# Optimization experiments

Hardware: AMD Instinct MI355X
Metric: run time of the kernel (lower is better)

## Reference

```python
import jax, jax.numpy as jnp
import numpy as np

N_NODES = 100000
N_EDGES = 1600000
D_IN = 128
D_OUT = 128


def setup_inputs() -> dict:
    key = jax.random.key(0)
    k1, k2, k3, k4, k5 = jax.random.split(key, 5)
    x = jax.random.normal(k1, (N_NODES, D_IN), dtype=jnp.float32)
    edge_row = jax.random.randint(k2, (N_EDGES,), 0, N_NODES, dtype=jnp.int32)
    edge_col = jax.random.randint(k3, (N_EDGES,), 0, N_NODES, dtype=jnp.int32)
    edge_vals = jax.random.uniform(k4, (N_EDGES,), dtype=jnp.float32)
    stdv = 1.0 / np.sqrt(D_OUT)
    weight = jax.random.uniform(k5, (D_IN, D_OUT), dtype=jnp.float32,
                                minval=-stdv, maxval=stdv)
    return {"x": x, "edge_row": edge_row, "edge_col": edge_col,
            "edge_vals": edge_vals, "weight": weight}


def reference(x, edge_row, edge_col, edge_vals, weight):
    # spmm(adj, x): gather source features, scale by edge weight, segment-sum to dst
    n = x.shape[0]
    msgs = x[edge_col] * edge_vals[:, None]          # [E, D_IN]
    agg = jax.ops.segment_sum(msgs, edge_row, num_segments=n)  # [N, D_IN]
    # dense weight matmul
    return agg @ weight                               # [N, D_OUT]
```

## Files before the change

### kernel.cpp

```cpp
#include <hip/hip_runtime.h>
#include <hip/hip_fp16.h>


#define N_NODES 100000
#define N_EDGES 1600000
#define DIM     128
#define BROWS   32
#define CB      3125
#define NSUP    49
#define LANES   8
#define NLR     (NSUP * LANES)
#define SLOT1   4608
#define SLOTCAP2 640
#define CAP     1024
#define OCAP    2048
#define CPAD    16

#define EPB1   1024
#define PBLK1  ((N_EDGES + EPB1 - 1) / EPB1)
#define CH2    1024
#define CPL    ((SLOT1 + CH2 - 1) / CH2)
#define PBLK2  (NLR * CPL)

#define OFF_CCUR1  25600000
#define OFF_CCUR2  25625088
#define OFF_OCNT   25825088
#define OFF_OBUF   25825152
#define OFF_EBUF1  25857920
#define OFF_EBUF2  40308608

__global__ __launch_bounds__(256) void gemm_xw_kernel(
    const float* __restrict__ x,
    const float* __restrict__ W,
    __half*      __restrict__ y)
{
    __shared__ __align__(16) float AsT[32 * 36];
    __shared__ float Ws[32 * 128];

    const int t    = threadIdx.x;
    const int row0 = blockIdx.x * 32;
    const int r0   = (t >> 5) * 4;
    const int c0   = (t & 31) * 4;

    float acc[4][4];
#pragma unroll
    for (int i = 0; i < 4; ++i)
#pragma unroll
        for (int j = 0; j < 4; ++j) acc[i][j] = 0.f;

    for (int k0 = 0; k0 < 128; k0 += 32) {
        {
            int r  = t >> 3;
            int kp = t & 7;
            float4 a = *(const float4*)(x + (size_t)(row0 + r) * 128 + k0 + kp * 4);
            AsT[(kp * 4 + 0) * 36 + r] = a.x;
            AsT[(kp * 4 + 1) * 36 + r] = a.y;
            AsT[(kp * 4 + 2) * 36 + r] = a.z;
            AsT[(kp * 4 + 3) * 36 + r] = a.w;
        }
        {
            const float4* Wg = (const float4*)(W + (size_t)k0 * 128);
            float4* Wl = (float4*)Ws;
#pragma unroll
            for (int i = 0; i < 4; ++i) Wl[t + 256 * i] = Wg[t + 256 * i];
        }
        __syncthreads();

#pragma unroll
        for (int kk = 0; kk < 32; ++kk) {
            float4 w = *(const float4*)(Ws + kk * 128 + c0);
            float4 a = *(const float4*)(AsT + kk * 36 + r0);
            acc[0][0] += a.x * w.x; acc[0][1] += a.x * w.y; acc[0][2] += a.x * w.z; acc[0][3] += a.x * w.w;
            acc[1][0] += a.y * w.x; acc[1][1] += a.y * w.y; acc[1][2] += a.y * w.z; acc[1][3] += a.y * w.w;
            acc[2][0] += a.z * w.x; acc[2][1] += a.z * w.y; acc[2][2] += a.z * w.z; acc[2][3] += a.z * w.w;
            acc[3][0] += a.w * w.x; acc[3][1] += a.w * w.y; acc[3][2] += a.w * w.z; acc[3][3] += a.w * w.w;
        }
        __syncthreads();
    }

#pragma unroll
    for (int i = 0; i < 4; ++i) {
        __half2 p0 = __floats2half2_rn(acc[i][0], acc[i][1]);
        __half2 p1 = __floats2half2_rn(acc[i][2], acc[i][3]);
        uint2 w;
        w.x = *(const unsigned*)&p0;
        w.y = *(const unsigned*)&p1;
        *(uint2*)(y + (size_t)(row0 + r0 + i) * 128 + c0) = w;
    }
}

__global__ __launch_bounds__(256) void zero_kernel(
    unsigned* ccur1, unsigned* ccur2, unsigned* ocnt)
{
    int i = blockIdx.x * 256 + threadIdx.x;
    if (i < NLR) ccur1[i * CPAD] = 0u;
    if (i < CB)  ccur2[i * CPAD] = 0u;
    if (i == 0)  *ocnt = 0u;
}

__global__ __launch_bounds__(256) void partition1_kernel(
    const int*   __restrict__ erow,
    const int*   __restrict__ ecol,
    const float* __restrict__ eval,
    unsigned*    __restrict__ ccur1,
    unsigned*    __restrict__ ocnt,
    uint4*       __restrict__ obuf,
    uint2*       __restrict__ ebuf1)
{
    __shared__ unsigned hist[NSUP];
    __shared__ unsigned gbase[NSUP];
    const int t = threadIdx.x;
    const unsigned e0   = blockIdx.x * (unsigned)EPB1;
    const unsigned lane = blockIdx.x & (LANES - 1);

    if (t < NSUP) hist[t] = 0u;
    __syncthreads();

    unsigned r[4], c[4], v[4]; bool ok[4];
#pragma unroll
    for (int k = 0; k < 4; ++k) {
        unsigned e = e0 + (unsigned)k * 256u + t;
        ok[k] = (e < N_EDGES);
        unsigned es = ok[k] ? e : (N_EDGES - 1);
        r[k] = (unsigned)erow[es];
        c[k] = (unsigned)ecol[es];
        v[k] = __float_as_uint(eval[es]);
    }
#pragma unroll
    for (int k = 0; k < 4; ++k)
        if (ok[k]) atomicAdd(&hist[r[k] >> 11], 1u);
    __syncthreads();

    if (t < NSUP) {
        unsigned h = hist[t];
        gbase[t] = h ? atomicAdd(&ccur1[(t * LANES + lane) * CPAD], h) : 0u;
        hist[t] = 0u;
    }
    __syncthreads();

#pragma unroll
    for (int k = 0; k < 4; ++k) {
        if (ok[k]) {
            unsigned s    = r[k] >> 11;
            unsigned rank = atomicAdd(&hist[s], 1u);
            unsigned slot = gbase[s] + rank;
            unsigned q    = s * LANES + lane;
            unsigned xw   = ((r[k] & 2047u) << 17) | c[k];
            if (slot < SLOT1) {
                ebuf1[(size_t)q * SLOT1 + slot] = make_uint2(xw, v[k]);
            } else {
                unsigned oi = atomicAdd(ocnt, 1u);
                if (oi < OCAP) obuf[oi] = make_uint4(xw, v[k], r[k] >> 5, 0u);
            }
        }
    }
}

__global__ __launch_bounds__(256) void partition2_kernel(
    const unsigned* __restrict__ ccur1,
    const uint2*    __restrict__ ebuf1,
    unsigned*       __restrict__ ccur2,
    unsigned*       __restrict__ ocnt,
    uint4*          __restrict__ obuf,
    uint2*          __restrict__ ebuf2)
{
    __shared__ unsigned hist[64];
    __shared__ unsigned gbase[64];
    const int t  = threadIdx.x;
    const int q  = blockIdx.x / CPL;
    const int ch = blockIdx.x % CPL;
    const int s  = q >> 3;

    unsigned cnt = ccur1[q * CPAD];
    if (cnt > SLOT1) cnt = SLOT1;
    const unsigned base = (unsigned)ch * CH2;
    if (base >= cnt) return;
    const unsigned m = (cnt - base < CH2) ? (cnt - base) : CH2;

    if (t < 64) hist[t] = 0u;
    __syncthreads();

    uint2 rec[4]; bool ok[4];
#pragma unroll
    for (int k = 0; k < 4; ++k) {
        unsigned idx = (unsigned)k * 256u + t;
        ok[k] = (idx < m);
        rec[k] = ok[k] ? ebuf1[(size_t)q * SLOT1 + base + idx] : make_uint2(0u, 0u);
    }
#pragma unroll
    for (int k = 0; k < 4; ++k)
        if (ok[k]) atomicAdd(&hist[(rec[k].x >> 22) & 63u], 1u);
    __syncthreads();

    if (t < 64) {
        unsigned h = hist[t];
        gbase[t] = h ? atomicAdd(&ccur2[(s * 64 + t) * CPAD], h) : 0u;
        hist[t] = 0u;
    }
    __syncthreads();

#pragma unroll
    for (int k = 0; k < 4; ++k) {
        if (ok[k]) {
            unsigned fin  = (rec[k].x >> 22) & 63u;
            unsigned rank = atomicAdd(&hist[fin], 1u);
            unsigned slot = gbase[fin] + rank;
            unsigned f    = (unsigned)s * 64u + fin;
            if (slot < SLOTCAP2) {
                ebuf2[(size_t)f * SLOTCAP2 + slot] = rec[k];
            } else {
                unsigned oi = atomicAdd(ocnt, 1u);
                if (oi < OCAP) obuf[oi] = make_uint4(rec[k].x, rec[k].y, f, 0u);
            }
        }
    }
}

__global__ __launch_bounds__(256) void bucket_agg_kernel(
    const __half*   __restrict__ y,
    const unsigned* __restrict__ ccur2,
    const unsigned* __restrict__ ocnt,
    const uint4*    __restrict__ obuf,
    const uint2*    __restrict__ ebuf2,
    float*          __restrict__ out)
{
    __shared__ uint2    raw[CAP];
    __shared__ uint2    sorted[CAP];
    __shared__ unsigned hist[BROWS];
    __shared__ unsigned sstart[BROWS];
    __shared__ unsigned scur[BROWS];
    __shared__ unsigned extn;

    const int t    = threadIdx.x;
    const int b    = blockIdx.x;
    const int lane = t & 63;
    const int wv   = t >> 6;

    const unsigned cnt = ccur2[b * CPAD];
    const unsigned n   = (cnt < SLOTCAP2) ? cnt : SLOTCAP2;
    const size_t   base = (size_t)b * SLOTCAP2;

    if (t == 0) extn = 0u;
    if (t < BROWS) hist[t] = 0u;
    __syncthreads();

    for (unsigned i = t; i < n; i += 256) {
        uint2 rec = ebuf2[base + i];
        raw[i] = rec;
        atomicAdd(&hist[(rec.x >> 17) & 31u], 1u);
    }

    unsigned oc = *ocnt;
    if (oc > OCAP) oc = OCAP;
    for (unsigned i = t; i < oc; i += 256) {
        uint4 o = obuf[i];
        if (o.z == (unsigned)b) {
            unsigned p = atomicAdd(&extn, 1u);
            if (n + p < CAP) {
                raw[n + p] = make_uint2(o.x, o.y);
                atomicAdd(&hist[(o.x >> 17) & 31u], 1u);
            }
        }
    }
    __syncthreads();

    unsigned m = n + extn;
    if (m > CAP) m = CAP;

    if (t < 64) {
        unsigned v = (t < BROWS) ? hist[t] : 0u;
        unsigned inc = v;
#pragma unroll
        for (int d = 1; d < 64; d <<= 1) {
            unsigned o = __shfl_up(inc, d);
            if (t >= d) inc += o;
        }
        unsigned excl = inc - v;
        if (t < BROWS) { sstart[t] = excl; scur[t] = excl; }
    }
    __syncthreads();

    for (unsigned i = t; i < m; i += 256) {
        uint2 rec = raw[i];
        unsigned p = atomicAdd(&scur[(rec.x >> 17) & 31u], 1u);
        sorted[p] = rec;
    }
    __syncthreads();

    for (int r = wv; r < BROWS; r += 4) {
        int row = b * BROWS + r;
        if (row >= N_NODES) break;
        float ax = 0.f, ay = 0.f;
        unsigned j = sstart[r], e = scur[r];
        for (; j + 4 <= e; j += 4) {
            uint2 r0 = sorted[j + 0];
            uint2 r1 = sorted[j + 1];
            uint2 r2 = sorted[j + 2];
            uint2 r3 = sorted[j + 3];
            const __half2 h0 = *((const __half2*)(y + (size_t)(r0.x & 0x1FFFFu) * 128) + lane);
            const __half2 h1 = *((const __half2*)(y + (size_t)(r1.x & 0x1FFFFu) * 128) + lane);
            const __half2 h2 = *((const __half2*)(y + (size_t)(r2.x & 0x1FFFFu) * 128) + lane);
            const __half2 h3 = *((const __half2*)(y + (size_t)(r3.x & 0x1FFFFu) * 128) + lane);
            float v0 = __uint_as_float(r0.y);
            float v1 = __uint_as_float(r1.y);
            float v2 = __uint_as_float(r2.y);
            float v3 = __uint_as_float(r3.y);
            float2 f0 = __half22float2(h0);
            float2 f1 = __half22float2(h1);
            float2 f2 = __half22float2(h2);
            float2 f3 = __half22float2(h3);
            ax = fmaf(f0.x, v0, ax); ay = fmaf(f0.y, v0, ay);
            ax = fmaf(f1.x, v1, ax); ay = fmaf(f1.y, v1, ay);
            ax = fmaf(f2.x, v2, ax); ay = fmaf(f2.y, v2, ay);
            ax = fmaf(f3.x, v3, ax); ay = fmaf(f3.y, v3, ay);
        }
        for (; j < e; ++j) {
            uint2 rr = sorted[j];
            const __half2 h = *((const __half2*)(y + (size_t)(rr.x & 0x1FFFFu) * 128) + lane);
            float v = __uint_as_float(rr.y);
            float2 f = __half22float2(h);
            ax = fmaf(f.x, v, ax); ay = fmaf(f.y, v, ay);
        }
        *((float2*)(out + (size_t)row * 128) + lane) = make_float2(ax, ay);
    }
}

extern "C" void kernel_launch(void* const* d_in, const int* in_sizes, int n_in,
                              void* d_out, int out_size, void* d_ws, size_t ws_size,
                              hipStream_t stream) {
    const float* x    = (const float*)d_in[0];
    const int*   erow = (const int*)d_in[1];
    const int*   ecol = (const int*)d_in[2];
    const float* eval = (const float*)d_in[3];
    const float* W    = (const float*)d_in[4];
    float* out = (float*)d_out;

    char* ws = (char*)d_ws;
    __half*   y     = (__half*)  (ws);
    unsigned* ccur1 = (unsigned*)(ws + OFF_CCUR1);
    unsigned* ccur2 = (unsigned*)(ws + OFF_CCUR2);
    unsigned* ocnt  = (unsigned*)(ws + OFF_OCNT);
    uint4*    obuf  = (uint4*)   (ws + OFF_OBUF);
    uint2*    ebuf1 = (uint2*)   (ws + OFF_EBUF1);
    uint2*    ebuf2 = (uint2*)   (ws + OFF_EBUF2);

    gemm_xw_kernel<<<N_NODES / 32, 256, 0, stream>>>(x, W, y);
    zero_kernel<<<(CB + 255) / 256, 256, 0, stream>>>(ccur1, ccur2, ocnt);
    partition1_kernel<<<PBLK1, 256, 0, stream>>>(erow, ecol, eval, ccur1, ocnt, obuf, ebuf1);
    partition2_kernel<<<PBLK2, 256, 0, stream>>>(ccur1, ebuf1, ccur2, ocnt, obuf, ebuf2);
    bucket_agg_kernel<<<CB, 256, 0, stream>>>(y, ccur2, ocnt, obuf, ebuf2, out);
}
```

Baseline: 235.9 us.

## Fuse XW GEMM and edge partition pass into one interleaved launch

Merges the dense x·W GEMM and the first edge-partition pass into a single kernel. Every third block computes a 128-row GEMM tile, now with 8x8 register tiles instead of 32-row, 4x4 tiles, and the other blocks do the partition work. The compute-bound GEMM and the memory/atomic-bound partition can then run concurrently on the GPU, and one launch is removed. The cost is heavier register and LDS use from the larger GEMM tile and the combined shared buffer, which may reduce occupancy for the partition blocks.

```diff
diff --git a/kernel.cpp b/kernel.cpp
--- a/kernel.cpp
+++ b/kernel.cpp
@@ -22,72 +22,15 @@
 #define CPL    ((SLOT1 + CH2 - 1) / CH2)
 #define PBLK2  (NLR * CPL)
 
+#define GBLK   782
+#define FBLK   (GBLK * 3)
+
 #define OFF_CCUR1  25600000
 #define OFF_CCUR2  25625088
 #define OFF_OCNT   25825088
 #define OFF_OBUF   25825152
 #define OFF_EBUF1  25857920
 #define OFF_EBUF2  40308608
-
-__global__ __launch_bounds__(256) void gemm_xw_kernel(
-    const float* __restrict__ x,
-    const float* __restrict__ W,
-    __half*      __restrict__ y)
-{
-    __shared__ __align__(16) float AsT[32 * 36];
-    __shared__ float Ws[32 * 128];
-
-    const int t    = threadIdx.x;
-    const int row0 = blockIdx.x * 32;
-    const int r0   = (t >> 5) * 4;
-    const int c0   = (t & 31) * 4;
-
-    float acc[4][4];
-#pragma unroll
-    for (int i = 0; i < 4; ++i)
-#pragma unroll
-        for (int j = 0; j < 4; ++j) acc[i][j] = 0.f;
-
-    for (int k0 = 0; k0 < 128; k0 += 32) {
-        {
-            int r  = t >> 3;
-            int kp = t & 7;
-            float4 a = *(const float4*)(x + (size_t)(row0 + r) * 128 + k0 + kp * 4);
-            AsT[(kp * 4 + 0) * 36 + r] = a.x;
-            AsT[(kp * 4 + 1) * 36 + r] = a.y;
-            AsT[(kp * 4 + 2) * 36 + r] = a.z;
-            AsT[(kp * 4 + 3) * 36 + r] = a.w;
-        }
-        {
-            const float4* Wg = (const float4*)(W + (size_t)k0 * 128);
-            float4* Wl = (float4*)Ws;
-#pragma unroll
-            for (int i = 0; i < 4; ++i) Wl[t + 256 * i] = Wg[t + 256 * i];
-        }
-        __syncthreads();
-
-#pragma unroll
-        for (int kk = 0; kk < 32; ++kk) {
-            float4 w = *(const float4*)(Ws + kk * 128 + c0);
-            float4 a = *(const float4*)(AsT + kk * 36 + r0);
-            acc[0][0] += a.x * w.x; acc[0][1] += a.x * w.y; acc[0][2] += a.x * w.z; acc[0][3] += a.x * w.w;
-            acc[1][0] += a.y * w.x; acc[1][1] += a.y * w.y; acc[1][2] += a.y * w.z; acc[1][3] += a.y * w.w;
-            acc[2][0] += a.z * w.x; acc[2][1] += a.z * w.y; acc[2][2] += a.z * w.z; acc[2][3] += a.z * w.w;
-            acc[3][0] += a.w * w.x; acc[3][1] += a.w * w.y; acc[3][2] += a.w * w.z; acc[3][3] += a.w * w.w;
-        }
-        __syncthreads();
-    }
-
-#pragma unroll
-    for (int i = 0; i < 4; ++i) {
-        __half2 p0 = __floats2half2_rn(acc[i][0], acc[i][1]);
-        __half2 p1 = __floats2half2_rn(acc[i][2], acc[i][3]);
-        uint2 w;
-        w.x = *(const unsigned*)&p0;
-        w.y = *(const unsigned*)&p1;
-        *(uint2*)(y + (size_t)(row0 + r0 + i) * 128 + c0) = w;
-    }
-}
 
 __global__ __launch_bounds__(256) void zero_kernel(
     unsigned* ccur1, unsigned* ccur2, unsigned* ocnt)
@@ -98,7 +41,10 @@
     if (i == 0)  *ocnt = 0u;
 }
 
-__global__ __launch_bounds__(256) void partition1_kernel(
+__global__ __launch_bounds__(256) void gemm_p1_kernel(
+    const float* __restrict__ x,
+    const float* __restrict__ W,
+    __half*      __restrict__ y,
     const int*   __restrict__ erow,
     const int*   __restrict__ ecol,
     const float* __restrict__ eval,
@@ -107,50 +53,127 @@
     uint4*       __restrict__ obuf,
     uint2*       __restrict__ ebuf1)
 {
-    __shared__ unsigned hist[NSUP];
-    __shared__ unsigned gbase[NSUP];
+    __shared__ __align__(16) char smem[33280];
+    const unsigned bid = blockIdx.x;
     const int t = threadIdx.x;
-    const unsigned e0   = blockIdx.x * (unsigned)EPB1;
-    const unsigned lane = blockIdx.x & (LANES - 1);
-
-    if (t < NSUP) hist[t] = 0u;
-    __syncthreads();
-
-    unsigned r[4], c[4], v[4]; bool ok[4];
-#pragma unroll
-    for (int k = 0; k < 4; ++k) {
-        unsigned e = e0 + (unsigned)k * 256u + t;
-        ok[k] = (e < N_EDGES);
-        unsigned es = ok[k] ? e : (N_EDGES - 1);
-        r[k] = (unsigned)erow[es];
-        c[k] = (unsigned)ecol[es];
-        v[k] = __float_as_uint(eval[es]);
-    }
-#pragma unroll
-    for (int k = 0; k < 4; ++k)
-        if (ok[k]) atomicAdd(&hist[r[k] >> 11], 1u);
-    __syncthreads();
-
-    if (t < NSUP) {
-        unsigned h = hist[t];
-        gbase[t] = h ? atomicAdd(&ccur1[(t * LANES + lane) * CPAD], h) : 0u;
-        hist[t] = 0u;
-    }
-    __syncthreads();
-
-#pragma unroll
-    for (int k = 0; k < 4; ++k) {
-        if (ok[k]) {
-            unsigned s    = r[k] >> 11;
-            unsigned rank = atomicAdd(&hist[s], 1u);
-            unsigned slot = gbase[s] + rank;
-            unsigned q    = s * LANES + lane;
-            unsigned xw   = ((r[k] & 2047u) << 17) | c[k];
-            if (slot < SLOT1) {
-                ebuf1[(size_t)q * SLOT1 + slot] = make_uint2(xw, v[k]);
-            } else {
-                unsigned oi = atomicAdd(ocnt, 1u);
-                if (oi < OCAP) obuf[oi] = make_uint4(xw, v[k], r[k] >> 5, 0u);
+
+    if (bid % 3u == 0u) {
+        float* AsT = (float*)smem;
+        float* Ws  = (float*)(smem + 16896);
+        const int g    = (int)(bid / 3u);
+        const int row0 = g * 128;
+        const int r0   = (t >> 4) * 8;
+        const int c0   = (t & 15) * 8;
+
+        float acc[8][8];
+#pragma unroll
+        for (int i = 0; i < 8; ++i)
+#pragma unroll
+            for (int j = 0; j < 8; ++j) acc[i][j] = 0.f;
+
+        for (int k0 = 0; k0 < 128; k0 += 32) {
+#pragma unroll
+            for (int i = 0; i < 4; ++i) {
+                int li = t + 256 * i;
+                int r  = li >> 3;
+                int kp = li & 7;
+                int grow = row0 + r;
+                float4 a = make_float4(0.f, 0.f, 0.f, 0.f);
+                if (grow < N_NODES)
+                    a = *(const float4*)(x + (size_t)grow * 128 + k0 + kp * 4);
+                AsT[(kp * 4 + 0) * 132 + r] = a.x;
+                AsT[(kp * 4 + 1) * 132 + r] = a.y;
+                AsT[(kp * 4 + 2) * 132 + r] = a.z;
+                AsT[(kp * 4 + 3) * 132 + r] = a.w;
+            }
+            {
+                const float4* Wg = (const float4*)(W + (size_t)k0 * 128);
+                float4* Wl = (float4*)Ws;
+#pragma unroll
+                for (int i = 0; i < 4; ++i) Wl[t + 256 * i] = Wg[t + 256 * i];
+            }
+            __syncthreads();
+
+#pragma unroll
+            for (int kk = 0; kk < 32; ++kk) {
+                float4 a0 = *(const float4*)(AsT + kk * 132 + r0);
+                float4 a1 = *(const float4*)(AsT + kk * 132 + r0 + 4);
+                float4 w0 = *(const float4*)(Ws  + kk * 128 + c0);
+                float4 w1 = *(const float4*)(Ws  + kk * 128 + c0 + 4);
+                float av[8] = { a0.x, a0.y, a0.z, a0.w, a1.x, a1.y, a1.z, a1.w };
+                float wv[8] = { w0.x, w0.y, w0.z, w0.w, w1.x, w1.y, w1.z, w1.w };
+#pragma unroll
+                for (int i = 0; i < 8; ++i)
+#pragma unroll
+                    for (int j = 0; j < 8; ++j)
+                        acc[i][j] = fmaf(av[i], wv[j], acc[i][j]);
+            }
+            __syncthreads();
+        }
+
+#pragma unroll
+        for (int i = 0; i < 8; ++i) {
+            int row = row0 + r0 + i;
+            if (row < N_NODES) {
+                __half2 p0 = __floats2half2_rn(acc[i][0], acc[i][1]);
+                __half2 p1 = __floats2half2_rn(acc[i][2], acc[i][3]);
+                __half2 p2 = __floats2half2_rn(acc[i][4], acc[i][5]);
+                __half2 p3 = __floats2half2_rn(acc[i][6], acc[i][7]);
+                uint4 w;
+                w.x = *(const unsigned*)&p0;
+                w.y = *(const unsigned*)&p1;
+                w.z = *(const unsigned*)&p2;
+                w.w = *(const unsigned*)&p3;
+                *(uint4*)(y + (size_t)row * 128 + c0) = w;
+            }
+        }
+    } else {
+        unsigned* hist  = (unsigned*)smem;
+        unsigned* gbase = hist + NSUP;
+        const unsigned pid = bid - 1u - (bid - 1u) / 3u;
+        if (pid >= PBLK1) return;
+        const unsigned e0   = pid * (unsigned)EPB1;
+        const unsigned lane = pid & (LANES - 1);
+
+        if (t < NSUP) hist[t] = 0u;
+        __syncthreads();
+
+        unsigned r[4], c[4], v[4]; bool ok[4];
+#pragma unroll
+        for (int k = 0; k < 4; ++k) {
+            unsigned e = e0 + (unsigned)k * 256u + t;
+            ok[k] = (e < N_EDGES);
+            unsigned es = ok[k] ? e : (N_EDGES - 1);
+            r[k] = (unsigned)erow[es];
+            c[k] = (unsigned)ecol[es];
+            v[k] = __float_as_uint(eval[es]);
+        }
+#pragma unroll
+        for (int k = 0; k < 4; ++k)
+            if (ok[k]) atomicAdd(&hist[r[k] >> 11], 1u);
+        __syncthreads();
+
+        if (t < NSUP) {
+            unsigned h = hist[t];
+            gbase[t] = h ? atomicAdd(&ccur1[(t * LANES + lane) * CPAD], h) : 0u;
+            hist[t] = 0u;
+        }
+        __syncthreads();
+
+#pragma unroll
+        for (int k = 0; k < 4; ++k) {
+            if (ok[k]) {
+                unsigned s    = r[k] >> 11;
+                unsigned rank = atomicAdd(&hist[s], 1u);
+                unsigned slot = gbase[s] + rank;
+                unsigned q    = s * LANES + lane;
+                unsigned xw   = ((r[k] & 2047u) << 17) | c[k];
+                if (slot < SLOT1) {
+                    ebuf1[(size_t)q * SLOT1 + slot] = make_uint2(xw, v[k]);
+                } else {
+                    unsigned oi = atomicAdd(ocnt, 1u);
+                    if (oi < OCAP) obuf[oi] = make_uint4(xw, v[k], r[k] >> 5, 0u);
+                }
             }
         }
     }
@@ -344,9 +367,9 @@
     uint2*    ebuf1 = (uint2*)   (ws + OFF_EBUF1);
     uint2*    ebuf2 = (uint2*)   (ws + OFF_EBUF2);
 
-    gemm_xw_kernel<<<N_NODES / 32, 256, 0, stream>>>(x, W, y);
     zero_kernel<<<(CB + 255) / 256, 256, 0, stream>>>(ccur1, ccur2, ocnt);
-    partition1_kernel<<<PBLK1, 256, 0, stream>>>(erow, ecol, eval, ccur1, ocnt, obuf, ebuf1);
+    gemm_p1_kernel<<<FBLK, 256, 0, stream>>>(x, W, y, erow, ecol, eval,
+                                             ccur1, ocnt, obuf, ebuf1);
     partition2_kernel<<<PBLK2, 256, 0, stream>>>(ccur1, ebuf1, ccur2, ocnt, obuf, ebuf2);
     bucket_agg_kernel<<<CB, 256, 0, stream>>>(y, ccur2, ocnt, obuf, ebuf2, out);
 }
```

Result: slower. 241.5 us (+2.4%).
